# Kernel optimization log

Hardware: AMD Instinct MI355X
Metric: run time of the kernel (lower is better)

The kernel has to match this reference:

```python
import jax, jax.numpy as jnp
import numpy as np

N_NODES = 50000
N_EDGES = 500000
N_REL = 8
D = 128        # input_dim
A_DIM = 64     # attention_dim
D_OUT = 128    # output_dim


def setup_inputs() -> dict:
    key = jax.random.key(0)
    ks = jax.random.split(key, 10)
    h = jax.random.normal(ks[0], (N_NODES, D), jnp.float32)
    # relation gate tables: [R, 2*D, D]; first D rows act on dst (subject), last D on src (object)
    relations = jax.random.normal(ks[1], (N_REL, 2 * D, D), jnp.float32) * 0.05
    rel_attention = jax.random.normal(ks[2], (N_REL, A_DIM), jnp.float32) * 0.05
    W_a = jax.random.normal(ks[3], (A_DIM, 2 * D), jnp.float32) * 0.05
    b_a = jnp.zeros((A_DIM,), jnp.float32)
    W_lin = jax.random.normal(ks[4], (D_OUT, 2 * D), jnp.float32) * 0.05
    b_lin = jnp.zeros((D_OUT,), jnp.float32)
    src = jax.random.randint(ks[5], (N_EDGES,), 0, N_NODES, dtype=jnp.int32)
    dst = jax.random.randint(ks[6], (N_EDGES,), 0, N_NODES, dtype=jnp.int32)
    etype = jax.random.randint(ks[7], (N_EDGES,), 0, N_REL, dtype=jnp.int32)
    return {"h": h, "relations": relations, "rel_attention": rel_attention,
            "W_a": W_a, "b_a": b_a, "W_lin": W_lin, "b_lin": b_lin,
            "src": src, "dst": dst, "etype": etype}


def reference(h, relations, rel_attention, W_a, b_a, W_lin, b_lin, src, dst, etype):
    d = h.shape[-1]
    # --- gates: relation-indexed gather_mm (concat gate type) ---
    # Project every node through every relation once (R is small), then gather per edge.
    proj_dst = jnp.einsum('nd,rde->rne', h, relations[:, :d, :])   # [R, N, D] subject/dst side
    proj_src = jnp.einsum('nd,rde->rne', h, relations[:, d:, :])   # [R, N, D] object/src side
    gate = jax.nn.sigmoid(proj_dst[etype, dst] + proj_src[etype, src])  # [E, D]

    src_h = h[src]   # [E, D]
    dst_h = h[dst]   # [E, D]

    # --- gatv2 attention (predicates are zeroed in the module -> rel_attention[0]) ---
    a = jax.nn.leaky_relu(jnp.concatenate([dst_h, src_h], axis=-1) @ W_a.T + b_a)  # [E, A]
    score = (rel_attention[0] * a).sum(-1)  # [E]

    # --- edge_softmax over destination-node segments ---
    smax = jax.ops.segment_max(score, dst, num_segments=N_NODES)
    ex = jnp.exp(score - smax[dst])
    denom = jax.ops.segment_sum(ex, dst, num_segments=N_NODES)
    attn = ex / denom[dst]  # [E]

    # --- message = u_mul_e(h, attn*gate), reduce = sum over dst ---
    msg = src_h * (attn[:, None] * gate)                 # [E, D]
    h_N = jax.ops.segment_sum(msg, dst, num_segments=N_NODES)  # [N, D]

    # --- graphsage aggregate: LeakyReLU(W [h ; h_N] + b) ---
    out = jax.nn.leaky_relu(jnp.concatenate([h, h_N], axis=-1) @ W_lin.T + b_lin)
    return out
```

## Files before the change

### kernel.cpp

```cpp
#include <hip/hip_runtime.h>
#include <cstdint>
#include <cstddef>

constexpr int NNODES = 50000;
constexpr int NEDGES = 500000;
constexpr int NRELS  = 8;
constexpr int DIM    = 128;
constexpr int ADIM   = 64;
constexpr int TWOD   = 256;
constexpr int EPB    = 64;
constexpr float SLOPE = 0.01f;

constexpr int XPITCH = TWOD + 8;
constexpr int SPAD = NEDGES + 1024;

typedef __attribute__((ext_vector_type(8))) short short8;
typedef __attribute__((ext_vector_type(4))) float floatx4;

__device__ __forceinline__ unsigned short f2bf(float f) {
    unsigned u = __float_as_uint(f);
    unsigned r = u + 0x7FFFu + ((u >> 16) & 1u);
    return (unsigned short)(r >> 16);
}
__device__ __forceinline__ float bf2f(unsigned short b) {
    return __uint_as_float(((unsigned)b) << 16);
}

__global__ void k_init(int4* __restrict__ sMeta, int* __restrict__ histD,
                       int* __restrict__ cursorD, int* __restrict__ cnts) {
    int i = blockIdx.x * blockDim.x + threadIdx.x;
    int stride = gridDim.x * blockDim.x;
    for (int idx = i; idx < SPAD; idx += stride) sMeta[idx] = make_int4(-1, 0, 0, 0);
    for (int idx = i; idx < NNODES; idx += stride) { histD[idx] = 0; cursorD[idx] = 0; }
    if (i < 16) cnts[i] = 0;
}

__global__ __launch_bounds__(256) void k_prep(const float* __restrict__ rel,
                                              const float* __restrict__ W_lin,
                                              const float* __restrict__ W_a,
                                              unsigned short* __restrict__ relT,
                                              unsigned short* __restrict__ Wl,
                                              unsigned short* __restrict__ Wa16) {
    __shared__ float ls[64][65];
    int b = blockIdx.x, t = threadIdx.x;
    if (b < 64) {
        int r = b >> 3, tile = b & 7;
        int d0 = (tile >> 1) * 64, o0 = (tile & 1) * 64;
        const float* rp = rel + ((size_t)r * TWOD + d0) * DIM + o0;
#pragma unroll
        for (int u = 0; u < 16; u++) {
            int v = u * 256 + t;
            int j = v & 63, i = v >> 6;
            ls[i][j] = rp[(size_t)i * DIM + j];
        }
        __syncthreads();
        unsigned short* wp = relT + ((size_t)r * DIM + o0) * TWOD + d0;
#pragma unroll
        for (int u = 0; u < 16; u++) {
            int v = u * 256 + t;
            int ii = v & 63, jj = v >> 6;
            wp[(size_t)jj * TWOD + ii] = f2bf(ls[ii][jj]);
        }
    } else {
        int idx = (b - 64) * 256 + t;
        if (idx < DIM * TWOD) {
            Wl[idx] = f2bf(W_lin[idx]);
        } else {
            int j = idx - DIM * TWOD;
            if (j < ADIM * TWOD) Wa16[j] = f2bf(W_a[j]);
        }
    }
}

__global__ void k_h16(const float* __restrict__ h, unsigned short* __restrict__ h16) {
    int i = blockIdx.x * 256 + threadIdx.x;
    if (i < NNODES * DIM / 8) {
        const float4* hp = (const float4*)(h + (size_t)i * 8);
        float4 a = hp[0], b = hp[1];
        union { unsigned short us[8]; short8 s8; } pk;
        pk.us[0] = f2bf(a.x); pk.us[1] = f2bf(a.y); pk.us[2] = f2bf(a.z); pk.us[3] = f2bf(a.w);
        pk.us[4] = f2bf(b.x); pk.us[5] = f2bf(b.y); pk.us[6] = f2bf(b.z); pk.us[7] = f2bf(b.w);
        *(short8*)&h16[(size_t)i * 8] = pk.s8;
    }
}

__global__ void k_hist2(const int* __restrict__ ety, const int* __restrict__ dst,
                        int* __restrict__ cnt, int* __restrict__ histD) {
    __shared__ int hist[NRELS];
    int t = threadIdx.x;
    if (t < NRELS) hist[t] = 0;
    __syncthreads();
    int e = blockIdx.x * 256 + t;
    if (e < NEDGES) {
        atomicAdd(&hist[ety[e]], 1);
        atomicAdd(&histD[dst[e]], 1);
    }
    __syncthreads();
    if (t < NRELS && hist[t] > 0) atomicAdd(&cnt[t], hist[t]);
}

__global__ __launch_bounds__(1024) void k_scan(const int* __restrict__ histD,
                                               int* __restrict__ row_ptr,
                                               const int* __restrict__ cnt,
                                               int* __restrict__ offs) {
    __shared__ int ls[1024];
    const int t = threadIdx.x;
    const int CH = (NNODES + 1023) / 1024;
    const int base = t * CH;
    int s = 0;
    for (int j = 0; j < CH; j++) { int i = base + j; if (i < NNODES) s += histD[i]; }
    ls[t] = s;
    __syncthreads();
    for (int off = 1; off < 1024; off <<= 1) {
        int v = (t >= off) ? ls[t - off] : 0;
        __syncthreads();
        ls[t] += v;
        __syncthreads();
    }
    int run = (t == 0) ? 0 : ls[t - 1];
    for (int j = 0; j < CH; j++) {
        int i = base + j;
        if (i < NNODES) { row_ptr[i] = run; run += histD[i]; }
    }
    if (t == 1023) row_ptr[NNODES] = ls[1023];
    if (t == 0) {
        int off = 0;
        for (int r = 0; r < NRELS; r++) {
            offs[r] = off;
            off += ((cnt[r] + EPB - 1) / EPB) * EPB;
        }
    }
}

__global__ void k_dscatter(const int* __restrict__ ety, const int* __restrict__ src,
                           const int* __restrict__ dst, const int* __restrict__ row_ptr,
                           int* __restrict__ cursorD, int4* __restrict__ meta4) {
    int e = blockIdx.x * 256 + threadIdx.x;
    if (e < NEDGES) {
        int dn = dst[e];
        int pos = row_ptr[dn] + atomicAdd(&cursorD[dn], 1);
        meta4[pos] = make_int4(src[e], dn, ety[e], 0);
    }
}

__global__ void k_scatter3(const int4* __restrict__ meta4, const int* __restrict__ offs,
                           int* __restrict__ cursorE, int4* __restrict__ sMeta) {
    __shared__ int hist[NRELS];
    __shared__ int basew[NRELS];
    int t = threadIdx.x;
    if (t < NRELS) hist[t] = 0;
    __syncthreads();
    int p = blockIdx.x * 256 + t;
    int r = -1, rank = 0;
    int4 m4 = make_int4(0, 0, 0, 0);
    if (p < NEDGES) {
        m4 = meta4[p];
        r = m4.z;
        rank = atomicAdd(&hist[r], 1);
    }
    __syncthreads();
    if (t < NRELS && hist[t] > 0) basew[t] = atomicAdd(&cursorE[t], hist[t]);
    __syncthreads();
    if (p < NEDGES) {
        int s = offs[r] + basew[r] + rank;
        sMeta[s] = make_int4(m4.x, m4.y, p, 0);
    }
}

__global__ __launch_bounds__(256) void k_gate_msg(
    const unsigned short* __restrict__ h16, const unsigned short* __restrict__ relT,
    const unsigned short* __restrict__ Wa16,
    const int4* __restrict__ sMeta, const float* __restrict__ b_a,
    const float* __restrict__ ratt, const int* __restrict__ offs,
    unsigned short* __restrict__ msgbuf, float* __restrict__ scoreP) {
    __shared__ unsigned short Xs[EPB * XPITCH];
    __shared__ int srcn_s[EPB];
    __shared__ int dstn_s[EPB];
    __shared__ int pos_s[EPB];
    __shared__ int val_s[EPB];
    __shared__ float scoreW[EPB][4];

    const int t = threadIdx.x;
    const int base = blockIdx.x * EPB;

    if (t < EPB) {
        int4 m4 = sMeta[base + t];
        int valid = m4.x >= 0;
        val_s[t] = valid;
        srcn_s[t] = valid ? m4.x : 0;
        dstn_s[t] = valid ? m4.y : 0;
        pos_s[t] = valid ? m4.z : 0;
    }
    __syncthreads();
    if (!val_s[0]) return;

    int r = 0;
#pragma unroll
    for (int i = 1; i < NRELS; i++) if (base >= offs[i]) r = i;

#pragma unroll
    for (int u = 0; u < 8; u++) {
        int v = u * 256 + t;
        int i = v >> 5;
        int c = v & 31;
        int node = (c < 16) ? dstn_s[i] : srcn_s[i];
        *(short8*)&Xs[i * XPITCH + c * 8] = *(const short8*)&h16[(size_t)node * DIM + (c & 15) * 8];
    }

    const int wave = t >> 6;
    const int lane = t & 63;
    const int q = lane >> 4;
    const int l16 = lane & 15;
    const int o16 = wave * 16 + l16;

    const unsigned short* bp0 = relT + ((size_t)r * DIM + (wave * 2 + 0) * 16 + l16) * TWOD + q * 8;
    const unsigned short* bp1 = relT + ((size_t)r * DIM + (wave * 2 + 1) * 16 + l16) * TWOD + q * 8;
    const unsigned short* wb  = Wa16 + (size_t)o16 * TWOD + q * 8;

    __syncthreads();

    floatx4 acc[4][2];
    floatx4 accS[4];
#pragma unroll
    for (int m = 0; m < 4; m++) {
        acc[m][0] = (floatx4)(0.0f);
        acc[m][1] = (floatx4)(0.0f);
        accS[m] = (floatx4)(0.0f);
    }

#pragma unroll
    for (int ks = 0; ks < 8; ks++) {
        short8 B0 = *(const short8*)(bp0 + ks * 32);
        short8 B1 = *(const short8*)(bp1 + ks * 32);
        short8 BS = *(const short8*)(wb + ks * 32);
        short8 Af[4];
        const unsigned short* xb = &Xs[l16 * XPITCH + ks * 32 + q * 8];
#pragma unroll
        for (int m = 0; m < 4; m++) Af[m] = *(const short8*)(xb + m * 16 * XPITCH);
#pragma unroll
        for (int m = 0; m < 4; m++) {
            acc[m][0] = __builtin_amdgcn_mfma_f32_16x16x32_bf16(Af[m], B0, acc[m][0], 0, 0, 0);
            acc[m][1] = __builtin_amdgcn_mfma_f32_16x16x32_bf16(Af[m], B1, acc[m][1], 0, 0, 0);
            accS[m]   = __builtin_amdgcn_mfma_f32_16x16x32_bf16(Af[m], BS, accS[m], 0, 0, 0);
        }
    }

    __syncthreads();

    {
        float ba = b_a[o16];
        float ra = ratt[o16];
#pragma unroll
        for (int m = 0; m < 4; m++) {
#pragma unroll
            for (int rg = 0; rg < 4; rg++) {
                float v = accS[m][rg] + ba;
                v = v > 0.0f ? v : SLOPE * v;
                v *= ra;
#pragma unroll
                for (int off = 8; off > 0; off >>= 1) v += __shfl_xor(v, off, 16);
                if (l16 == 0) scoreW[m * 16 + q * 4 + rg][wave] = v;
            }
        }
    }

#pragma unroll
    for (int m = 0; m < 4; m++) {
        int ib = m * 16 + q * 4;
#pragma unroll
        for (int nn = 0; nn < 2; nn++) {
            int o = (wave * 2 + nn) * 16 + l16;
#pragma unroll
            for (int rg = 0; rg < 4; rg++) {
                int i = ib + rg;
                float g = 1.0f / (1.0f + __expf(-acc[m][nn][rg]));
                float sh = bf2f(Xs[i * XPITCH + DIM + o]);
                Xs[i * XPITCH + o] = f2bf(sh * g);
            }
        }
    }
    __syncthreads();

#pragma unroll
    for (int u = 0; u < 4; u++) {
        int v = u * 256 + t;
        int i = v >> 4;
        int c = v & 15;
        if (!val_s[i]) continue;
        short8 val = *(const short8*)&Xs[i * XPITCH + c * 8];
        *(short8*)&msgbuf[(size_t)pos_s[i] * DIM + c * 8] = val;
    }
    if (t < EPB && val_s[t]) {
        scoreP[pos_s[t]] = scoreW[t][0] + scoreW[t][1] + scoreW[t][2] + scoreW[t][3];
    }
}

__global__ __launch_bounds__(256) void k_segsoft(float* __restrict__ scoreP,
                                                 const int* __restrict__ row_ptr) {
    int n = blockIdx.x * 16 + (threadIdx.x >> 4);
    int l = threadIdx.x & 15;
    if (n >= NNODES) return;
    int p0 = row_ptr[n], p1 = row_ptr[n + 1];
    if (p0 >= p1) return;
    float m = -3.0e38f;
    for (int p = p0 + l; p < p1; p += 16) m = fmaxf(m, scoreP[p]);
#pragma unroll
    for (int off = 8; off > 0; off >>= 1) m = fmaxf(m, __shfl_xor(m, off, 16));
    float sum = 0.0f;
    for (int p = p0 + l; p < p1; p += 16) {
        float x = __expf(scoreP[p] - m);
        scoreP[p] = x;
        sum += x;
    }
#pragma unroll
    for (int off = 8; off > 0; off >>= 1) sum += __shfl_xor(sum, off, 16);
    float inv = 1.0f / sum;
    for (int p = p0 + l; p < p1; p += 16) scoreP[p] *= inv;
}

__global__ __launch_bounds__(256) void k_aggr(const unsigned short* __restrict__ msgbuf,
                                              const float* __restrict__ attP,
                                              const int* __restrict__ row_ptr,
                                              unsigned short* __restrict__ hN16) {
    int n = blockIdx.x * 4 + (threadIdx.x >> 6);
    int lane = threadIdx.x & 63;
    if (n >= NNODES) return;
    int p0 = row_ptr[n], p1 = row_ptr[n + 1];
    float a0 = 0.0f, a1 = 0.0f;
    for (int p = p0; p < p1; p++) {
        float at = attP[p];
        unsigned v = *(const unsigned*)&msgbuf[(size_t)p * DIM + lane * 2];
        a0 += at * bf2f((unsigned short)(v & 0xFFFFu));
        a1 += at * bf2f((unsigned short)(v >> 16));
    }
    unsigned o = (unsigned)f2bf(a0) | ((unsigned)f2bf(a1) << 16);
    *(unsigned*)&hN16[(size_t)n * DIM + lane * 2] = o;
}

__global__ __launch_bounds__(256) void k_out(const unsigned short* __restrict__ h16,
                                             const unsigned short* __restrict__ hN16,
                                             const unsigned short* __restrict__ Wl,
                                             const float* __restrict__ b_lin,
                                             float* __restrict__ out) {
    __shared__ unsigned short Xs[EPB * XPITCH];
    const int t = threadIdx.x;
    const int nb = blockIdx.x * 64;

#pragma unroll
    for (int u = 0; u < 8; u++) {
        int v = u * 256 + t;
        int i = v >> 5;
        int c = v & 31;
        int n = nb + i;
        if (n >= NNODES) n = NNODES - 1;
        const unsigned short* srcp = (c < 16) ? h16 : hN16;
        *(short8*)&Xs[i * XPITCH + c * 8] = *(const short8*)&srcp[(size_t)n * DIM + (c & 15) * 8];
    }

    const int wave = t >> 6;
    const int lane = t & 63;
    const int q = lane >> 4;
    const int l16 = lane & 15;

    short8 Bf[2][8];
#pragma unroll
    for (int nn = 0; nn < 2; nn++) {
        int o = (wave * 2 + nn) * 16 + l16;
        const unsigned short* bp = Wl + (size_t)o * TWOD + q * 8;
#pragma unroll
        for (int ks = 0; ks < 8; ks++) Bf[nn][ks] = *(const short8*)(bp + ks * 32);
    }

    __syncthreads();

    floatx4 acc[4][2];
#pragma unroll
    for (int m = 0; m < 4; m++)
#pragma unroll
        for (int nn = 0; nn < 2; nn++) acc[m][nn] = (floatx4)(0.0f);

#pragma unroll
    for (int ks = 0; ks < 8; ks++) {
        short8 Af[4];
        const unsigned short* xb = &Xs[l16 * XPITCH + ks * 32 + q * 8];
#pragma unroll
        for (int m = 0; m < 4; m++) Af[m] = *(const short8*)(xb + m * 16 * XPITCH);
#pragma unroll
        for (int m = 0; m < 4; m++)
#pragma unroll
            for (int nn = 0; nn < 2; nn++)
                acc[m][nn] = __builtin_amdgcn_mfma_f32_16x16x32_bf16(Af[m], Bf[nn][ks], acc[m][nn], 0, 0, 0);
    }

#pragma unroll
    for (int m = 0; m < 4; m++) {
        int ib = m * 16 + q * 4;
#pragma unroll
        for (int nn = 0; nn < 2; nn++) {
            int o = (wave * 2 + nn) * 16 + l16;
            float bl = b_lin[o];
#pragma unroll
            for (int rg = 0; rg < 4; rg++) {
                int n = nb + ib + rg;
                if (n < NNODES) {
                    float val = acc[m][nn][rg] + bl;
                    val = val > 0.0f ? val : SLOPE * val;
                    out[(size_t)n * DIM + o] = val;
                }
            }
        }
    }
}

extern "C" void kernel_launch(void* const* d_in, const int* in_sizes, int n_in,
                              void* d_out, int out_size, void* d_ws, size_t ws_size,
                              hipStream_t stream) {
    const float* h     = (const float*)d_in[0];
    const float* rel   = (const float*)d_in[1];
    const float* ratt  = (const float*)d_in[2];
    const float* W_a   = (const float*)d_in[3];
    const float* b_a   = (const float*)d_in[4];
    const float* W_lin = (const float*)d_in[5];
    const float* b_lin = (const float*)d_in[6];
    const int* src = (const int*)d_in[7];
    const int* dst = (const int*)d_in[8];
    const int* ety = (const int*)d_in[9];
    float* out = (float*)d_out;

    float* scoreP = (float*)d_ws;
    unsigned short* h16  = (unsigned short*)(scoreP + NEDGES);
    unsigned short* hN16 = h16 + (size_t)NNODES * DIM;
    unsigned short* relT = hN16 + (size_t)NNODES * DIM;
    unsigned short* Wl   = relT + (size_t)NRELS * DIM * TWOD;
    unsigned short* Wa16 = Wl + (size_t)DIM * TWOD;
    int4* meta4  = (int4*)(Wa16 + (size_t)ADIM * TWOD);
    int4* sMeta  = meta4 + NEDGES;
    int* row_ptr = (int*)(sMeta + SPAD);
    int* histD   = row_ptr + (NNODES + 1);
    int* cursorD = histD + NNODES;
    int* cnts    = cursorD + NNODES;
    int* offs    = cnts + 16;
    unsigned short* msgbuf = (unsigned short*)(((uintptr_t)(offs + 8) + 255) & ~(uintptr_t)255);

    k_init<<<2048, 256, 0, stream>>>(sMeta, histD, cursorD, cnts);
    k_prep<<<64 + (DIM * TWOD + ADIM * TWOD + 255) / 256, 256, 0, stream>>>(
        rel, W_lin, W_a, relT, Wl, Wa16);
    k_h16<<<(NNODES * DIM / 8 + 255) / 256, 256, 0, stream>>>(h, h16);
    k_hist2<<<(NEDGES + 255) / 256, 256, 0, stream>>>(ety, dst, cnts, histD);
    k_scan<<<1, 1024, 0, stream>>>(histD, row_ptr, cnts, offs);
    k_dscatter<<<(NEDGES + 255) / 256, 256, 0, stream>>>(
        ety, src, dst, row_ptr, cursorD, meta4);
    k_scatter3<<<(NEDGES + 255) / 256, 256, 0, stream>>>(meta4, offs, cnts + 8, sMeta);
    k_gate_msg<<<(NEDGES + 8 * EPB + EPB - 1) / EPB, 256, 0, stream>>>(
        h16, relT, Wa16, sMeta, b_a, ratt, offs, msgbuf, scoreP);
    k_segsoft<<<(NNODES + 15) / 16, 256, 0, stream>>>(scoreP, row_ptr);
    k_aggr<<<(NNODES + 3) / 4, 256, 0, stream>>>(msgbuf, scoreP, row_ptr, hN16);
    k_out<<<(NNODES + 63) / 64, 256, 0, stream>>>(h16, hN16, Wl, b_lin, out);
}
```

Before: 475.3 us.

## Fuse edge softmax, aggregation and output GEMM; pack edge metadata into 8 bytes

Merges the segment softmax, the per-node weighted aggregation and the final linear layer into one kernel. Aggregated neighbour features now go straight into shared memory instead of a global hN16 buffer, which removes two launches and the hN16 write and reread. Edge metadata shrinks from int4 to uint2, with src and dst packed as 16-bit halves, to cut scatter traffic. In exchange, one wave now handles 16 nodes serially with scalar softmax loops, so there is less parallelism per node. The 16-bit packing only holds while node ids stay below 65536.

```diff
diff --git a/kernel.cpp b/kernel.cpp
--- a/kernel.cpp
+++ b/kernel.cpp
@@ -26,11 +26,11 @@
     return __uint_as_float(((unsigned)b) << 16);
 }
 
-__global__ void k_init(int4* __restrict__ sMeta, int* __restrict__ histD,
+__global__ void k_init(uint2* __restrict__ sMeta, int* __restrict__ histD,
                        int* __restrict__ cursorD, int* __restrict__ cnts) {
     int i = blockIdx.x * blockDim.x + threadIdx.x;
     int stride = gridDim.x * blockDim.x;
-    for (int idx = i; idx < SPAD; idx += stride) sMeta[idx] = make_int4(-1, 0, 0, 0);
+    for (int idx = i; idx < SPAD; idx += stride) sMeta[idx] = make_uint2(0xFFFFFFFFu, 0u);
     for (int idx = i; idx < NNODES; idx += stride) { histD[idx] = 0; cursorD[idx] = 0; }
     if (i < 16) cnts[i] = 0;
 }
@@ -134,17 +134,17 @@
 
 __global__ void k_dscatter(const int* __restrict__ ety, const int* __restrict__ src,
                            const int* __restrict__ dst, const int* __restrict__ row_ptr,
-                           int* __restrict__ cursorD, int4* __restrict__ meta4) {
+                           int* __restrict__ cursorD, uint2* __restrict__ meta2) {
     int e = blockIdx.x * 256 + threadIdx.x;
     if (e < NEDGES) {
         int dn = dst[e];
         int pos = row_ptr[dn] + atomicAdd(&cursorD[dn], 1);
-        meta4[pos] = make_int4(src[e], dn, ety[e], 0);
-    }
-}
-
-__global__ void k_scatter3(const int4* __restrict__ meta4, const int* __restrict__ offs,
-                           int* __restrict__ cursorE, int4* __restrict__ sMeta) {
+        meta2[pos] = make_uint2((unsigned)src[e] | ((unsigned)dn << 16), (unsigned)ety[e]);
+    }
+}
+
+__global__ void k_scatter3(const uint2* __restrict__ meta2, const int* __restrict__ offs,
+                           int* __restrict__ cursorE, uint2* __restrict__ sMeta) {
     __shared__ int hist[NRELS];
     __shared__ int basew[NRELS];
     int t = threadIdx.x;
@@ -152,10 +152,10 @@
     __syncthreads();
     int p = blockIdx.x * 256 + t;
     int r = -1, rank = 0;
-    int4 m4 = make_int4(0, 0, 0, 0);
+    uint2 m2 = make_uint2(0u, 0u);
     if (p < NEDGES) {
-        m4 = meta4[p];
-        r = m4.z;
+        m2 = meta2[p];
+        r = (int)m2.y;
         rank = atomicAdd(&hist[r], 1);
     }
     __syncthreads();
@@ -163,14 +163,14 @@
     __syncthreads();
     if (p < NEDGES) {
         int s = offs[r] + basew[r] + rank;
-        sMeta[s] = make_int4(m4.x, m4.y, p, 0);
+        sMeta[s] = make_uint2(m2.x, (unsigned)p);
     }
 }
 
 __global__ __launch_bounds__(256) void k_gate_msg(
     const unsigned short* __restrict__ h16, const unsigned short* __restrict__ relT,
     const unsigned short* __restrict__ Wa16,
-    const int4* __restrict__ sMeta, const float* __restrict__ b_a,
+    const uint2* __restrict__ sMeta, const float* __restrict__ b_a,
     const float* __restrict__ ratt, const int* __restrict__ offs,
     unsigned short* __restrict__ msgbuf, float* __restrict__ scoreP) {
     __shared__ unsigned short Xs[EPB * XPITCH];
@@ -184,12 +184,12 @@
     const int base = blockIdx.x * EPB;
 
     if (t < EPB) {
-        int4 m4 = sMeta[base + t];
-        int valid = m4.x >= 0;
+        uint2 m2 = sMeta[base + t];
+        int valid = (m2.x != 0xFFFFFFFFu);
         val_s[t] = valid;
-        srcn_s[t] = valid ? m4.x : 0;
-        dstn_s[t] = valid ? m4.y : 0;
-        pos_s[t] = valid ? m4.z : 0;
+        srcn_s[t] = valid ? (int)(m2.x & 0xFFFFu) : 0;
+        dstn_s[t] = valid ? (int)(m2.x >> 16) : 0;
+        pos_s[t] = valid ? (int)m2.y : 0;
     }
     __syncthreads();
     if (!val_s[0]) return;
@@ -295,70 +295,51 @@
     }
 }
 
-__global__ __launch_bounds__(256) void k_segsoft(float* __restrict__ scoreP,
-                                                 const int* __restrict__ row_ptr) {
-    int n = blockIdx.x * 16 + (threadIdx.x >> 4);
-    int l = threadIdx.x & 15;
-    if (n >= NNODES) return;
-    int p0 = row_ptr[n], p1 = row_ptr[n + 1];
-    if (p0 >= p1) return;
-    float m = -3.0e38f;
-    for (int p = p0 + l; p < p1; p += 16) m = fmaxf(m, scoreP[p]);
-#pragma unroll
-    for (int off = 8; off > 0; off >>= 1) m = fmaxf(m, __shfl_xor(m, off, 16));
-    float sum = 0.0f;
-    for (int p = p0 + l; p < p1; p += 16) {
-        float x = __expf(scoreP[p] - m);
-        scoreP[p] = x;
-        sum += x;
-    }
-#pragma unroll
-    for (int off = 8; off > 0; off >>= 1) sum += __shfl_xor(sum, off, 16);
-    float inv = 1.0f / sum;
-    for (int p = p0 + l; p < p1; p += 16) scoreP[p] *= inv;
-}
-
-__global__ __launch_bounds__(256) void k_aggr(const unsigned short* __restrict__ msgbuf,
-                                              const float* __restrict__ attP,
-                                              const int* __restrict__ row_ptr,
-                                              unsigned short* __restrict__ hN16) {
-    int n = blockIdx.x * 4 + (threadIdx.x >> 6);
-    int lane = threadIdx.x & 63;
-    if (n >= NNODES) return;
-    int p0 = row_ptr[n], p1 = row_ptr[n + 1];
-    float a0 = 0.0f, a1 = 0.0f;
-    for (int p = p0; p < p1; p++) {
-        float at = attP[p];
-        unsigned v = *(const unsigned*)&msgbuf[(size_t)p * DIM + lane * 2];
-        a0 += at * bf2f((unsigned short)(v & 0xFFFFu));
-        a1 += at * bf2f((unsigned short)(v >> 16));
-    }
-    unsigned o = (unsigned)f2bf(a0) | ((unsigned)f2bf(a1) << 16);
-    *(unsigned*)&hN16[(size_t)n * DIM + lane * 2] = o;
-}
-
-__global__ __launch_bounds__(256) void k_out(const unsigned short* __restrict__ h16,
-                                             const unsigned short* __restrict__ hN16,
-                                             const unsigned short* __restrict__ Wl,
-                                             const float* __restrict__ b_lin,
-                                             float* __restrict__ out) {
+__global__ __launch_bounds__(256) void k_aggr_out(
+    const unsigned short* __restrict__ h16, const unsigned short* __restrict__ msgbuf,
+    const float* __restrict__ scoreP, const int* __restrict__ row_ptr,
+    const unsigned short* __restrict__ Wl, const float* __restrict__ b_lin,
+    float* __restrict__ out) {
     __shared__ unsigned short Xs[EPB * XPITCH];
     const int t = threadIdx.x;
     const int nb = blockIdx.x * 64;
-
-#pragma unroll
-    for (int u = 0; u < 8; u++) {
+    const int wave = t >> 6;
+    const int lane = t & 63;
+
+    for (int j = 0; j < 16; j++) {
+        int i = wave * 16 + j;
+        int n = nb + i;
+        float a0 = 0.0f, a1 = 0.0f;
+        if (n < NNODES) {
+            int p0 = row_ptr[n], p1 = row_ptr[n + 1];
+            if (p0 < p1) {
+                float mx = -3.0e38f;
+                for (int p = p0; p < p1; p++) mx = fmaxf(mx, scoreP[p]);
+                float sum = 0.0f;
+                for (int p = p0; p < p1; p++) sum += __expf(scoreP[p] - mx);
+                float inv = 1.0f / sum;
+                for (int p = p0; p < p1; p++) {
+                    float w = __expf(scoreP[p] - mx) * inv;
+                    unsigned v = *(const unsigned*)&msgbuf[(size_t)p * DIM + lane * 2];
+                    a0 += w * bf2f((unsigned short)(v & 0xFFFFu));
+                    a1 += w * bf2f((unsigned short)(v >> 16));
+                }
+            }
+        }
+        unsigned o = (unsigned)f2bf(a0) | ((unsigned)f2bf(a1) << 16);
+        *(unsigned*)&Xs[i * XPITCH + DIM + lane * 2] = o;
+    }
+
+#pragma unroll
+    for (int u = 0; u < 4; u++) {
         int v = u * 256 + t;
-        int i = v >> 5;
-        int c = v & 31;
+        int i = v >> 4;
+        int c = v & 15;
         int n = nb + i;
         if (n >= NNODES) n = NNODES - 1;
-        const unsigned short* srcp = (c < 16) ? h16 : hN16;
-        *(short8*)&Xs[i * XPITCH + c * 8] = *(const short8*)&srcp[(size_t)n * DIM + (c & 15) * 8];
-    }
-
-    const int wave = t >> 6;
-    const int lane = t & 63;
+        *(short8*)&Xs[i * XPITCH + c * 8] = *(const short8*)&h16[(size_t)n * DIM + c * 8];
+    }
+
     const int q = lane >> 4;
     const int l16 = lane & 15;
 
@@ -429,12 +410,11 @@
 
     float* scoreP = (float*)d_ws;
     unsigned short* h16  = (unsigned short*)(scoreP + NEDGES);
-    unsigned short* hN16 = h16 + (size_t)NNODES * DIM;
-    unsigned short* relT = hN16 + (size_t)NNODES * DIM;
+    unsigned short* relT = h16 + (size_t)NNODES * DIM;
     unsigned short* Wl   = relT + (size_t)NRELS * DIM * TWOD;
     unsigned short* Wa16 = Wl + (size_t)DIM * TWOD;
-    int4* meta4  = (int4*)(Wa16 + (size_t)ADIM * TWOD);
-    int4* sMeta  = meta4 + NEDGES;
+    uint2* meta2 = (uint2*)(Wa16 + (size_t)ADIM * TWOD);
+    uint2* sMeta = meta2 + NEDGES;
     int* row_ptr = (int*)(sMeta + SPAD);
     int* histD   = row_ptr + (NNODES + 1);
     int* cursorD = histD + NNODES;
@@ -449,11 +429,10 @@
     k_hist2<<<(NEDGES + 255) / 256, 256, 0, stream>>>(ety, dst, cnts, histD);
     k_scan<<<1, 1024, 0, stream>>>(histD, row_ptr, cnts, offs);
     k_dscatter<<<(NEDGES + 255) / 256, 256, 0, stream>>>(
-        ety, src, dst, row_ptr, cursorD, meta4);
-    k_scatter3<<<(NEDGES + 255) / 256, 256, 0, stream>>>(meta4, offs, cnts + 8, sMeta);
+        ety, src, dst, row_ptr, cursorD, meta2);
+    k_scatter3<<<(NEDGES + 255) / 256, 256, 0, stream>>>(meta2, offs, cnts + 8, sMeta);
     k_gate_msg<<<(NEDGES + 8 * EPB + EPB - 1) / EPB, 256, 0, stream>>>(
         h16, relT, Wa16, sMeta, b_a, ratt, offs, msgbuf, scoreP);
-    k_segsoft<<<(NNODES + 15) / 16, 256, 0, stream>>>(scoreP, row_ptr);
-    k_aggr<<<(NNODES + 3) / 4, 256, 0, stream>>>(msgbuf, scoreP, row_ptr, hN16);
-    k_out<<<(NNODES + 63) / 64, 256, 0, stream>>>(h16, hN16, Wl, b_lin, out);
-}
+    k_aggr_out<<<(NNODES + 63) / 64, 256, 0, stream>>>(
+        h16, msgbuf, scoreP, row_ptr, Wl, b_lin, out);
+}
```

After: 663.1 us. 39.5% more time.
